# Kernel tuning notes

Hardware: AMD Instinct MI355X
Metric: run time of the kernel (lower is better)

Reference implementation:

```python
import jax, jax.numpy as jnp
import numpy as np

N, C, H, E = 4096, 512, 8, 131072
D = C // H
ALPHA = 0.5
EPS = 1e-5


def layer_norm(x, g, b):
    mu = jnp.mean(x, axis=-1, keepdims=True)
    var = jnp.mean((x - mu) ** 2, axis=-1, keepdims=True)
    return (x - mu) * jax.lax.rsqrt(var + EPS) * g + b


def setup_inputs() -> dict:
    key = jax.random.key(0)
    ks = jax.random.split(key, 20)
    s = 0.02
    return {
        "x": jax.random.normal(ks[0], (N, C), jnp.float32),
        "edge_index": jax.random.randint(ks[1], (2, E), 0, N, jnp.int32),
        "local_w": jax.random.normal(ks[2], (C, C), jnp.float32) * s,
        "local_b": jnp.zeros((C,), jnp.float32),
        "in_proj_w": jax.random.normal(ks[3], (3 * C, C), jnp.float32) * s,
        "in_proj_b": jnp.zeros((3 * C,), jnp.float32),
        "attn_out_w": jax.random.normal(ks[4], (C, C), jnp.float32) * s,
        "attn_out_b": jnp.zeros((C,), jnp.float32),
        "output_w": jax.random.normal(ks[5], (C, C), jnp.float32) * s,
        "output_b": jnp.zeros((C,), jnp.float32),
        "norm1_g": jnp.ones((C,), jnp.float32),
        "norm1_b": jnp.zeros((C,), jnp.float32),
        "norm2_g": jnp.ones((C,), jnp.float32),
        "norm2_b": jnp.zeros((C,), jnp.float32),
        "ffn_w1": jax.random.normal(ks[6], (2 * C, C), jnp.float32) * s,
        "ffn_b1": jnp.zeros((2 * C,), jnp.float32),
        "ffn_w2": jax.random.normal(ks[7], (C, 2 * C), jnp.float32) * s,
        "ffn_b2": jnp.zeros((C,), jnp.float32),
    }


def reference(x, edge_index, local_w, local_b, in_proj_w, in_proj_b,
              attn_out_w, attn_out_b, output_w, output_b,
              norm1_g, norm1_b, norm2_g, norm2_b,
              ffn_w1, ffn_b1, ffn_w2, ffn_b2):
    src, dst = edge_index[0], edge_index[1]

    # local branch: linear then scatter-mean over incoming edges
    local_h = x @ local_w.T + local_b                       # [N,C]
    summed = jax.ops.segment_sum(local_h[src], dst, num_segments=N)
    cnt = jax.ops.segment_sum(jnp.ones((E,), x.dtype), dst, num_segments=N)
    local_out = summed / jnp.maximum(cnt, 1.0)[:, None]

    # global branch: full self-attention over all nodes
    qkv = x @ in_proj_w.T + in_proj_b                       # [N,3C]
    q, k, v = jnp.split(qkv, 3, axis=-1)
    q = q.reshape(N, H, D)
    k = k.reshape(N, H, D)
    v = v.reshape(N, H, D)
    scores = jnp.einsum('nhd,mhd->hnm', q, k) / jnp.sqrt(jnp.asarray(D, x.dtype))
    attn = jax.nn.softmax(scores, axis=-1)                  # [H,N,N]
    ctx = jnp.einsum('hnm,mhd->nhd', attn, v).reshape(N, C)
    global_out = ctx @ attn_out_w.T + attn_out_b

    mixed = ALPHA * local_out + (1.0 - ALPHA) * global_out
    hidden = layer_norm(x + (mixed @ output_w.T + output_b), norm1_g, norm1_b)

    ff = jax.nn.gelu(hidden @ ffn_w1.T + ffn_b1, approximate=False) @ ffn_w2.T + ffn_b2
    return layer_norm(hidden + ff, norm2_g, norm2_b)
```

## Files before the change

kernel.cpp:

```cpp
#include <hip/hip_runtime.h>


#define N_NODES 4096
#define C_DIM   512
#define H_HEADS 8
#define D_HEAD  64
#define E_EDGES 131072

typedef unsigned short u16;
typedef unsigned int   u32;
typedef u16   u16x8  __attribute__((ext_vector_type(8)));
typedef __bf16 bf16x8 __attribute__((ext_vector_type(8)));
typedef float  f32x4  __attribute__((ext_vector_type(4)));

__device__ __forceinline__ float b2f(u16 u) {
  unsigned int i = ((unsigned int)u) << 16;
  return __builtin_bit_cast(float, i);
}
__device__ __forceinline__ u16 f2b(float f) {
  unsigned int i = __builtin_bit_cast(unsigned int, f);
  i += 0x7fffu + ((i >> 16) & 1u);
  return (u16)(i >> 16);
}
__device__ __forceinline__ u16 f2b_up(float f) {
  unsigned int i = __builtin_bit_cast(unsigned int, f);
  return (u16)((i + 0x8000u) >> 16);
}
__device__ __forceinline__ void glds16(const u16* g, u16* l) {
  __builtin_amdgcn_global_load_lds(
      (const __attribute__((address_space(1))) void*)g,
      (__attribute__((address_space(3))) void*)l, 16, 0, 0);
}

struct CvtArgs {
  const float* src[7];
  u16* dst[7];
  int n[7];
  const int* ei;
  int* deg;
};

__global__ __launch_bounds__(256) void cvt_multi(CvtArgs a) {
  const int t = blockIdx.y;
  if (t == 7) {
    if (blockIdx.x >= E_EDGES / 256) return;
    const int e = blockIdx.x * 256 + threadIdx.x;
    atomicAdd(&a.deg[a.ei[E_EDGES + e]], 1);
    return;
  }
  const int i = (blockIdx.x * 256 + threadIdx.x) * 8;
  if (i >= a.n[t]) return;
  const float* s = a.src[t] + i;
  f32x4 v0 = *(const f32x4*)s;
  f32x4 v1 = *(const f32x4*)(s + 4);
  u16x8 o;
  o[0]=f2b(v0[0]); o[1]=f2b(v0[1]); o[2]=f2b(v0[2]); o[3]=f2b(v0[3]);
  o[4]=f2b(v1[0]); o[5]=f2b(v1[1]); o[6]=f2b(v1[2]); o[7]=f2b(v1[3]);
  *(u16x8*)(a.dst[t] + i) = o;
}

template<int EPI>
__global__ __launch_bounds__(256) void gemm_bt(
    const u16* __restrict__ A, const u16* __restrict__ W,
    const float* __restrict__ bias, void* __restrict__ outp,
    int M, int Nout, int K,
    const float* __restrict__ mloc)
{
  const int tid  = threadIdx.x;
  const int lane = tid & 63, wave = tid >> 6;
  const int quad = lane >> 4, l16 = lane & 15;
  const int wm = wave >> 1, wn = wave & 1;
  const int bm = blockIdx.x, bnb = blockIdx.y;

  __shared__ __align__(16) u16 As[64][128];
  __shared__ __align__(16) u16 Ws[64][128];

  f32x4 acc[2][2] = {};

  const int lr4 = lane >> 4, gs = lane & 15;
  const int g8e = (gs ^ lr4) * 8;
  const int g8o = (gs ^ (4 + lr4)) * 8;
  const u16* aw[8];
#pragma unroll
  for (int c = 0; c < 4; ++c) {
    const int g8 = (c & 1) ? g8o : g8e;
    aw[c]     = A + (size_t)(bm  * 64 + wave * 16 + c * 4 + lr4) * K + g8;
    aw[4 + c] = W + (size_t)(bnb * 64 + wave * 16 + c * 4 + lr4) * K + g8;
  }

  for (int k0 = 0; k0 < K; k0 += 128) {
    __syncthreads();
#pragma unroll
    for (int c = 0; c < 4; ++c) {
      glds16(aw[c] + k0,     &As[wave * 16 + c * 4][0]);
      glds16(aw[4 + c] + k0, &Ws[wave * 16 + c * 4][0]);
    }
    __syncthreads();
#pragma unroll
    for (int ks = 0; ks < 4; ++ks) {
      const int slot = ((ks * 4 + quad) ^ (l16 & 7)) * 8;
      bf16x8 af[2], bf[2];
      af[0] = *(const bf16x8*)&As[wm * 32 +      l16][slot];
      af[1] = *(const bf16x8*)&As[wm * 32 + 16 + l16][slot];
      bf[0] = *(const bf16x8*)&Ws[wn * 32 +      l16][slot];
      bf[1] = *(const bf16x8*)&Ws[wn * 32 + 16 + l16][slot];
#pragma unroll
      for (int i = 0; i < 2; ++i)
#pragma unroll
        for (int j = 0; j < 2; ++j)
          acc[i][j] = __builtin_amdgcn_mfma_f32_16x16x32_bf16(af[i], bf[j], acc[i][j], 0, 0, 0);
    }
  }

#pragma unroll
  for (int i = 0; i < 2; ++i)
#pragma unroll
    for (int j = 0; j < 2; ++j) {
      const int col = bnb * 64 + wn * 32 + j * 16 + l16;
      const float bias_v = bias[col];
#pragma unroll
      for (int r = 0; r < 4; ++r) {
        const int row = bm * 64 + wm * 32 + i * 16 + quad * 4 + r;
        float v = acc[i][j][r] + bias_v;
        const size_t o = (size_t)row * Nout + col;
        if constexpr (EPI == 1) {
          ((float*)outp)[o] = v;
        } else if constexpr (EPI == 2) {
          float gl = 0.5f * v * (1.0f + erff(v * 0.70710678118654752f));
          ((u16*)outp)[o] = f2b(gl);
        } else {
          ((u16*)outp)[o] = f2b(0.5f * mloc[o] + 0.5f * v);
        }
      }
    }
}

__global__ __launch_bounds__(256) void gemm128(
    const u16* __restrict__ A, const u16* __restrict__ W,
    const float* __restrict__ bias0, const float* __restrict__ bias1,
    u16* __restrict__ out0, u16* __restrict__ out1,
    int M, int Nout, int K)
{
  const int tid  = threadIdx.x;
  const int lane = tid & 63, wave = tid >> 6;
  const int quad = lane >> 4, l16 = lane & 15;
  const int wm = wave >> 1, wn = wave & 1;
  const int bm = blockIdx.x, bnb = blockIdx.y;

  __shared__ __align__(16) u16 As[128][64];
  __shared__ __align__(16) u16 Ws[128][64];

  f32x4 acc[4][4] = {};

  const int lr = lane >> 3, gs = lane & 7;
  const int g8 = (gs ^ lr) * 8;
  const u16* ab = A + (size_t)(bm  * 128 + wave * 32 + lr) * K + g8;
  const u16* wb = W + (size_t)(bnb * 128 + wave * 32 + lr) * K + g8;

  for (int k0 = 0; k0 < K; k0 += 64) {
    __syncthreads();
#pragma unroll
    for (int c = 0; c < 4; ++c) {
      glds16(ab + (size_t)(c * 8) * K + k0, &As[wave * 32 + c * 8][0]);
      glds16(wb + (size_t)(c * 8) * K + k0, &Ws[wave * 32 + c * 8][0]);
    }
    __syncthreads();
#pragma unroll
    for (int ks = 0; ks < 2; ++ks) {
      const int slot = ((ks * 4 + quad) ^ (l16 & 7)) * 8;
      bf16x8 af[4], bf[4];
#pragma unroll
      for (int am = 0; am < 4; ++am)
        af[am] = *(const bf16x8*)&As[wm * 64 + am * 16 + l16][slot];
#pragma unroll
      for (int bn = 0; bn < 4; ++bn)
        bf[bn] = *(const bf16x8*)&Ws[wn * 64 + bn * 16 + l16][slot];
#pragma unroll
      for (int am = 0; am < 4; ++am)
#pragma unroll
        for (int bn = 0; bn < 4; ++bn)
          acc[am][bn] = __builtin_amdgcn_mfma_f32_16x16x32_bf16(af[am], bf[bn], acc[am][bn], 0, 0, 0);
    }
  }

#pragma unroll
  for (int am = 0; am < 4; ++am)
#pragma unroll
    for (int bn = 0; bn < 4; ++bn) {
      const int col = bnb * 128 + wn * 64 + bn * 16 + l16;
      const float bias_v = (col < 512) ? bias0[col] : bias1[col - 512];
#pragma unroll
      for (int r = 0; r < 4; ++r) {
        const int row = bm * 128 + wm * 64 + am * 16 + quad * 4 + r;
        float v = acc[am][bn][r] + bias_v;
        if (col < 512) out0[(size_t)row * 512 + col] = f2b(v);
        else           out1[(size_t)row * 1536 + (col - 512)] = f2b(v);
      }
    }
}

__global__ __launch_bounds__(256) void scan_kernel(
    const int* __restrict__ deg, int* __restrict__ off, int* __restrict__ cursor)
{
  __shared__ int part[256];
  const int t = threadIdx.x;
  int v[16];
  int s = 0;
#pragma unroll
  for (int i = 0; i < 16; ++i) { v[i] = deg[t * 16 + i]; s += v[i]; }
  part[t] = s;
  __syncthreads();
  for (int d = 1; d < 256; d <<= 1) {
    int val = (t >= d) ? part[t - d] : 0;
    __syncthreads();
    if (t >= d) part[t] += val;
    __syncthreads();
  }
  int prefix = (t == 0) ? 0 : part[t - 1];
#pragma unroll
  for (int i = 0; i < 16; ++i) {
    off[t * 16 + i] = prefix;
    cursor[t * 16 + i] = prefix;
    prefix += v[i];
  }
  if (t == 255) off[4096] = prefix;
}

__global__ __launch_bounds__(256) void fill_kernel(
    const int* __restrict__ ei, int* __restrict__ cursor, int* __restrict__ csr)
{
  const int e = blockIdx.x * 256 + threadIdx.x;
  const int s = ei[e];
  const int d = ei[E_EDGES + e];
  const int p = atomicAdd(&cursor[d], 1);
  csr[p] = s;
}

__global__ __launch_bounds__(256) void gather_vtrans(
    const int* __restrict__ off, const int* __restrict__ csr,
    const u16* __restrict__ lh, float* __restrict__ lo,
    const u16* __restrict__ qkv, u16* __restrict__ vt)
{
  if (blockIdx.y == 0) {
    const int wave = threadIdx.x >> 6, lane = threadIdx.x & 63;
    const int n = blockIdx.x * 4 + wave;
    const int j0 = off[n], j1 = off[n + 1];
    float acc[8] = {};
    for (int j = j0; j < j1; ++j) {
      const int s = csr[j];
      const u16x8 v = *(const u16x8*)(lh + (size_t)s * C_DIM + lane * 8);
#pragma unroll
      for (int i = 0; i < 8; ++i) acc[i] += b2f(v[i]);
    }
    const float inv = 1.0f / fmaxf((float)(j1 - j0), 1.0f);
    f32x4 o0, o1;
#pragma unroll
    for (int i = 0; i < 4; ++i) { o0[i] = acc[i] * inv; o1[i] = acc[4 + i] * inv; }
    float* op = lo + (size_t)n * C_DIM + lane * 8;
    *(f32x4*)op = o0;
    *(f32x4*)(op + 4) = o1;
  } else {
    if (blockIdx.x >= 512) return;
    const int tid = threadIdx.x;
    const int d = tid & 63, mg = tid >> 6;
    const int h = blockIdx.x >> 6, mt = blockIdx.x & 63;
    const int m0 = mt * 64 + mg * 16;
    u16 buf[16];
#pragma unroll
    for (int i = 0; i < 16; ++i)
      buf[i] = qkv[(size_t)(m0 + i) * 1536 + 1024 + h * 64 + d];
    u16x8 w0, w1;
#pragma unroll
    for (int i = 0; i < 8; ++i) { w0[i] = buf[i]; w1[i] = buf[8 + i]; }
    u16* op = vt + (size_t)(h * 64 + d) * N_NODES + m0;
    *(u16x8*)op = w0;
    *(u16x8*)(op + 8) = w1;
  }
}

template<int SPLITS>
__global__ __launch_bounds__(256) void attn_kernel(
    const u16* __restrict__ qkv, const u16* __restrict__ vt,
    u16* __restrict__ opart, float* __restrict__ lpart)
{
  const int tid = threadIdx.x, wave = tid >> 6, lane = tid & 63;
  const int quad = lane >> 4, l16 = lane & 15;
  const int h = blockIdx.y, tile = blockIdx.x, split = blockIdx.z;

  __shared__ __align__(16) u16 Ks[64][64];
  __shared__ __align__(16) u16 Vts[64][64];
  __shared__ __align__(16) u16 Ps[128][72];

  const float QSCALE = 0.18033688011112042f;
  bf16x8 aq[2][2];
#pragma unroll
  for (int mb = 0; mb < 2; ++mb) {
    const int qrow = tile * 128 + wave * 32 + mb * 16 + l16;
    const u16* qp = qkv + (size_t)qrow * 1536 + h * 64 + quad * 8;
    u16x8 q0 = *(const u16x8*)qp;
    u16x8 q1 = *(const u16x8*)(qp + 32);
    u16x8 s0, s1;
#pragma unroll
    for (int i = 0; i < 8; ++i) {
      s0[i] = f2b(b2f(q0[i]) * QSCALE);
      s1[i] = f2b(b2f(q1[i]) * QSCALE);
    }
    aq[mb][0] = __builtin_bit_cast(bf16x8, s0);
    aq[mb][1] = __builtin_bit_cast(bf16x8, s1);
  }

  f32x4 O[2][4] = {};
  float lsum[2][4] = {};

  const int lr = lane >> 3, gs = lane & 7;
  const int g8 = (gs ^ lr) * 8;
  const int R0 = wave * 16 + lr;

  const int mt1 = (split + 1) * (64 / SPLITS);
  for (int mt = split * (64 / SPLITS); mt < mt1; ++mt) {
    __syncthreads();
    glds16(qkv + (size_t)(mt * 64 + R0)     * 1536 + 512 + h * 64 + g8, &Ks[wave * 16][0]);
    glds16(qkv + (size_t)(mt * 64 + R0 + 8) * 1536 + 512 + h * 64 + g8, &Ks[wave * 16 + 8][0]);
    glds16(vt + (size_t)(h * 64 + R0)     * N_NODES + mt * 64 + g8, &Vts[wave * 16][0]);
    glds16(vt + (size_t)(h * 64 + R0 + 8) * N_NODES + mt * 64 + g8, &Vts[wave * 16 + 8][0]);
    __syncthreads();

    f32x4 s[2][4] = {};
#pragma unroll
    for (int ks = 0; ks < 2; ++ks) {
      const int slot = ((ks * 4 + quad) ^ (l16 & 7)) * 8;
      bf16x8 bk[4];
#pragma unroll
      for (int jn = 0; jn < 4; ++jn)
        bk[jn] = *(const bf16x8*)&Ks[jn * 16 + l16][slot];
#pragma unroll
      for (int mb = 0; mb < 2; ++mb)
#pragma unroll
        for (int jn = 0; jn < 4; ++jn)
          s[mb][jn] = __builtin_amdgcn_mfma_f32_16x16x32_bf16(aq[mb][ks], bk[jn], s[mb][jn], 0, 0, 0);
    }

#pragma unroll
    for (int mb = 0; mb < 2; ++mb)
#pragma unroll
      for (int jn = 0; jn < 4; ++jn)
#pragma unroll
        for (int r = 0; r < 4; ++r) {
          float p = __builtin_amdgcn_exp2f(s[mb][jn][r]);
          lsum[mb][r] += p;
          Ps[wave * 32 + mb * 16 + quad * 4 + r][jn * 16 + l16] = f2b_up(p);
        }

#pragma unroll
    for (int ks = 0; ks < 2; ++ks) {
      const int slot = ((ks * 4 + quad) ^ (l16 & 7)) * 8;
      bf16x8 bv[4];
#pragma unroll
      for (int jd = 0; jd < 4; ++jd)
        bv[jd] = *(const bf16x8*)&Vts[jd * 16 + l16][slot];
#pragma unroll
      for (int mb = 0; mb < 2; ++mb) {
        bf16x8 ap = *(const bf16x8*)&Ps[wave * 32 + mb * 16 + l16][ks * 32 + quad * 8];
#pragma unroll
        for (int jd = 0; jd < 4; ++jd)
          O[mb][jd] = __builtin_amdgcn_mfma_f32_16x16x32_bf16(ap, bv[jd], O[mb][jd], 0, 0, 0);
      }
    }
  }

#pragma unroll
  for (int mb = 0; mb < 2; ++mb)
#pragma unroll
    for (int r = 0; r < 4; ++r)
#pragma unroll
      for (int off = 1; off < 16; off <<= 1)
        lsum[mb][r] += __shfl_xor(lsum[mb][r], off);

#pragma unroll
  for (int mb = 0; mb < 2; ++mb)
#pragma unroll
    for (int r = 0; r < 4; ++r) {
      const int row = tile * 128 + wave * 32 + mb * 16 + quad * 4 + r;
      u16* orow = opart + ((size_t)split * N_NODES + row) * C_DIM + h * 64;
#pragma unroll
      for (int jd = 0; jd < 4; ++jd)
        orow[jd * 16 + l16] = f2b(O[mb][jd][r]);
      if (l16 == 0)
        lpart[((size_t)split * N_NODES + row) * H_HEADS + h] = lsum[mb][r];
    }
}

template<int SPLITS>
__global__ __launch_bounds__(256) void attn_combine(
    const u16* __restrict__ opart, const float* __restrict__ lpart,
    u16* __restrict__ ctx)
{
  const size_t base = (size_t)(blockIdx.x * 256 + threadIdx.x) * 8;
  const int row = (int)(base >> 9);
  const int h = (int)((base & 511) >> 6);
  float l = 0.0f;
#pragma unroll
  for (int s = 0; s < SPLITS; ++s)
    l += lpart[(size_t)s * N_NODES * H_HEADS + (size_t)row * H_HEADS + h];
  const float inv = 1.0f / l;
  float o[8] = {};
#pragma unroll
  for (int s = 0; s < SPLITS; ++s) {
    const u16x8 p = *(const u16x8*)(opart + (size_t)s * N_NODES * C_DIM + base);
#pragma unroll
    for (int i = 0; i < 8; ++i) o[i] += b2f(p[i]);
  }
  u16x8 ob;
#pragma unroll
  for (int i = 0; i < 8; ++i) ob[i] = f2b(o[i] * inv);
  *(u16x8*)(ctx + base) = ob;
}

__global__ __launch_bounds__(256) void ln1_kernel(
    const float* __restrict__ x, const float* __restrict__ pr,
    const float* __restrict__ g, const float* __restrict__ b,
    u16* __restrict__ hb, float* __restrict__ hf)
{
  const int wave = threadIdx.x >> 6, lane = threadIdx.x & 63;
  const int row = blockIdx.x * 4 + wave;
  const int c0 = lane * 8;
  const size_t base = (size_t)row * C_DIM + c0;
  f32x4 x0 = *(const f32x4*)(x + base);
  f32x4 x1 = *(const f32x4*)(x + base + 4);
  f32x4 p0 = *(const f32x4*)(pr + base);
  f32x4 p1 = *(const f32x4*)(pr + base + 4);
  float v[8];
#pragma unroll
  for (int i = 0; i < 4; ++i) { v[i] = x0[i] + p0[i]; v[4 + i] = x1[i] + p1[i]; }
  float sum = 0, sq = 0;
#pragma unroll
  for (int i = 0; i < 8; ++i) { sum += v[i]; sq += v[i] * v[i]; }
  for (int off = 1; off < 64; off <<= 1) { sum += __shfl_xor(sum, off); sq += __shfl_xor(sq, off); }
  const float mean = sum * (1.0f / C_DIM);
  const float var  = sq * (1.0f / C_DIM) - mean * mean;
  const float rstd = rsqrtf(var + 1e-5f);
  f32x4 g0 = *(const f32x4*)(g + c0), g1 = *(const f32x4*)(g + c0 + 4);
  f32x4 b0 = *(const f32x4*)(b + c0), b1 = *(const f32x4*)(b + c0 + 4);
  u16x8 ob; f32x4 h0, h1;
#pragma unroll
  for (int i = 0; i < 4; ++i) {
    float hv0 = (v[i]     - mean) * rstd * g0[i] + b0[i];
    float hv1 = (v[4 + i] - mean) * rstd * g1[i] + b1[i];
    h0[i] = hv0; h1[i] = hv1;
    ob[i] = f2b(hv0); ob[4 + i] = f2b(hv1);
  }
  *(u16x8*)(hb + base) = ob;
  *(f32x4*)(hf + base) = h0;
  *(f32x4*)(hf + base + 4) = h1;
}

__global__ __launch_bounds__(256) void ln2_kernel(
    const float* __restrict__ a, const float* __restrict__ c,
    const float* __restrict__ g, const float* __restrict__ b,
    float* __restrict__ out)
{
  const int wave = threadIdx.x >> 6, lane = threadIdx.x & 63;
  const int row = blockIdx.x * 4 + wave;
  const int c0 = lane * 8;
  const size_t base = (size_t)row * C_DIM + c0;
  f32x4 a0 = *(const f32x4*)(a + base), a1 = *(const f32x4*)(a + base + 4);
  f32x4 c0v = *(const f32x4*)(c + base), c1v = *(const f32x4*)(c + base + 4);
  float v[8];
#pragma unroll
  for (int i = 0; i < 4; ++i) { v[i] = a0[i] + c0v[i]; v[4 + i] = a1[i] + c1v[i]; }
  float sum = 0, sq = 0;
#pragma unroll
  for (int i = 0; i < 8; ++i) { sum += v[i]; sq += v[i] * v[i]; }
  for (int off = 1; off < 64; off <<= 1) { sum += __shfl_xor(sum, off); sq += __shfl_xor(sq, off); }
  const float mean = sum * (1.0f / C_DIM);
  const float var  = sq * (1.0f / C_DIM) - mean * mean;
  const float rstd = rsqrtf(var + 1e-5f);
  f32x4 g0 = *(const f32x4*)(g + c0), g1 = *(const f32x4*)(g + c0 + 4);
  f32x4 b0 = *(const f32x4*)(b + c0), b1 = *(const f32x4*)(b + c0 + 4);
  f32x4 h0, h1;
#pragma unroll
  for (int i = 0; i < 4; ++i) {
    h0[i] = (v[i]     - mean) * rstd * g0[i] + b0[i];
    h1[i] = (v[4 + i] - mean) * rstd * g1[i] + b1[i];
  }
  *(f32x4*)(out + base) = h0;
  *(f32x4*)(out + base + 4) = h1;
}

extern "C" void kernel_launch(void* const* d_in, const int* in_sizes, int n_in,
                              void* d_out, int out_size, void* d_ws, size_t ws_size,
                              hipStream_t stream) {
  const float* x          = (const float*)d_in[0];
  const int*   ei         = (const int*)d_in[1];
  const float* local_w    = (const float*)d_in[2];
  const float* local_b    = (const float*)d_in[3];
  const float* in_proj_w  = (const float*)d_in[4];
  const float* in_proj_b  = (const float*)d_in[5];
  const float* attn_out_w = (const float*)d_in[6];
  const float* attn_out_b = (const float*)d_in[7];
  const float* output_w   = (const float*)d_in[8];
  const float* output_b   = (const float*)d_in[9];
  const float* n1g = (const float*)d_in[10];
  const float* n1b = (const float*)d_in[11];
  const float* n2g = (const float*)d_in[12];
  const float* n2b = (const float*)d_in[13];
  const float* ffn_w1 = (const float*)d_in[14];
  const float* ffn_b1 = (const float*)d_in[15];
  const float* ffn_w2 = (const float*)d_in[16];
  const float* ffn_b2 = (const float*)d_in[17];
  float* out = (float*)d_out;

  char* ws = (char*)d_ws;
  size_t o = 0;
  float* local_out = (float*)(ws + o); o += (size_t)N_NODES * C_DIM * 4;
  int* deg    = (int*)(ws + o); o += (N_NODES) * 4;
  int* off    = (int*)(ws + o); o += (N_NODES + 16) * 4;
  int* cursor = (int*)(ws + o); o += (N_NODES) * 4;
  int* csr    = (int*)(ws + o); o += (size_t)E_EDGES * 4;
  u16* xb   = (u16*)(ws + o); o += (size_t)N_NODES * C_DIM * 2;
  u16* wbLQ = (u16*)(ws + o); o += (size_t)4 * C_DIM * C_DIM * 2;
  u16* wbA  = (u16*)(ws + o); o += (size_t)C_DIM * C_DIM * 2;
  u16* wbO  = (u16*)(ws + o); o += (size_t)C_DIM * C_DIM * 2;
  u16* wbF1 = (u16*)(ws + o); o += (size_t)2 * C_DIM * C_DIM * 2;
  u16* wbF2 = (u16*)(ws + o); o += (size_t)2 * C_DIM * C_DIM * 2;
  u16* local_h   = (u16*)(ws + o); o += (size_t)N_NODES * C_DIM * 2;
  u16* qkvb      = (u16*)(ws + o); o += (size_t)N_NODES * 3 * C_DIM * 2;
  u16* ctxb      = (u16*)(ws + o); o += (size_t)N_NODES * C_DIM * 2;
  u16* mixed     = (u16*)(ws + o); o += (size_t)N_NODES * C_DIM * 2;
  u16* hidden_bf = (u16*)(ws + o); o += (size_t)N_NODES * C_DIM * 2;
  float* hidden_f = (float*)(ws + o); o += (size_t)N_NODES * C_DIM * 4;
  u16* ff1       = (u16*)(ws + o); o += (size_t)N_NODES * 2 * C_DIM * 2;
  float* proj  = (float*)qkvb;
  float* ff2   = (float*)local_out;
  u16*   vt    = xb;
  u16* opart4 = (u16*)(ws + o);
  float* lpart4 = (float*)(ws + o + (size_t)4 * N_NODES * C_DIM * 2);
  const size_t need4 = o + (size_t)4 * N_NODES * C_DIM * 2 + (size_t)4 * N_NODES * H_HEADS * 4;
  const bool use4 = (ws_size >= need4);
  u16* opart2 = (u16*)hidden_bf;
  float* lpart2 = (float*)(opart2 + (size_t)2 * N_NODES * C_DIM);

  (void)hipMemsetAsync(deg, 0, N_NODES * 4, stream);

  CvtArgs ca;
  ca.src[0] = x;          ca.dst[0] = xb;   ca.n[0] = N_NODES * C_DIM;
  ca.src[1] = local_w;    ca.dst[1] = wbLQ;                  ca.n[1] = C_DIM * C_DIM;
  ca.src[2] = in_proj_w;  ca.dst[2] = wbLQ + C_DIM * C_DIM;  ca.n[2] = 3 * C_DIM * C_DIM;
  ca.src[3] = attn_out_w; ca.dst[3] = wbA;  ca.n[3] = C_DIM * C_DIM;
  ca.src[4] = output_w;   ca.dst[4] = wbO;  ca.n[4] = C_DIM * C_DIM;
  ca.src[5] = ffn_w1;     ca.dst[5] = wbF1; ca.n[5] = 2 * C_DIM * C_DIM;
  ca.src[6] = ffn_w2;     ca.dst[6] = wbF2; ca.n[6] = 2 * C_DIM * C_DIM;
  ca.ei = ei; ca.deg = deg;
  cvt_multi<<<dim3(N_NODES * C_DIM / 2048, 8), 256, 0, stream>>>(ca);

  scan_kernel<<<1, 256, 0, stream>>>(deg, off, cursor);
  fill_kernel<<<E_EDGES / 256, 256, 0, stream>>>(ei, cursor, csr);

  gemm128<<<dim3(32, 16), 256, 0, stream>>>(xb, wbLQ, local_b, in_proj_b,
      local_h, qkvb, N_NODES, 4 * C_DIM, C_DIM);

  gather_vtrans<<<dim3(N_NODES / 4, 2), 256, 0, stream>>>(off, csr, local_h,
      local_out, qkvb, vt);

  if (use4) {
    attn_kernel<4><<<dim3(32, 8, 4), 256, 0, stream>>>(qkvb, vt, opart4, lpart4);
    attn_combine<4><<<N_NODES * C_DIM / 2048, 256, 0, stream>>>(opart4, lpart4, ctxb);
  } else {
    attn_kernel<2><<<dim3(32, 8, 2), 256, 0, stream>>>(qkvb, vt, opart2, lpart2);
    attn_combine<2><<<N_NODES * C_DIM / 2048, 256, 0, stream>>>(opart2, lpart2, ctxb);
  }

  gemm_bt<3><<<dim3(64, 8), 256, 0, stream>>>(ctxb, wbA, attn_out_b, mixed,
      N_NODES, C_DIM, C_DIM, local_out);

  gemm_bt<1><<<dim3(64, 8), 256, 0, stream>>>(mixed, wbO, output_b, proj,
      N_NODES, C_DIM, C_DIM, nullptr);
  ln1_kernel<<<N_NODES / 4, 256, 0, stream>>>(x, proj, n1g, n1b, hidden_bf, hidden_f);

  gemm_bt<2><<<dim3(64, 16), 256, 0, stream>>>(hidden_bf, wbF1, ffn_b1, ff1,
      N_NODES, 2 * C_DIM, C_DIM, nullptr);
  gemm_bt<1><<<dim3(64, 8), 256, 0, stream>>>(ff1, wbF2, ffn_b2, ff2,
      N_NODES, C_DIM, 2 * C_DIM, nullptr);
  ln2_kernel<<<N_NODES / 4, 256, 0, stream>>>(hidden_f, ff2, n2g, n2b, out);
}
```

Measured before the change: 272.1 us.

## Fold graph CSR build into GEMM, vtrans and attention kernels to cut launches

Moves the degree counting into extra blocks of the QKV GEMM, merges the prefix scan with the V transpose, moves the CSR fill into extra blocks of the attention kernel, and fuses the neighbour gather with the attention combine. The deg memset becomes a block in the conversion kernel. The aim is to drop several small kernel launches and the memset, and to hide the latency-bound graph work behind the large kernels. In exchange the atomic-heavy blocks now compete with the GEMM and attention blocks for the same GPU.

```diff
diff --git a/kernel.cpp b/kernel.cpp
--- a/kernel.cpp
+++ b/kernel.cpp
@@ -36,16 +36,14 @@
   const float* src[7];
   u16* dst[7];
   int n[7];
-  const int* ei;
   int* deg;
 };
 
 __global__ __launch_bounds__(256) void cvt_multi(CvtArgs a) {
   const int t = blockIdx.y;
   if (t == 7) {
-    if (blockIdx.x >= E_EDGES / 256) return;
-    const int e = blockIdx.x * 256 + threadIdx.x;
-    atomicAdd(&a.deg[a.ei[E_EDGES + e]], 1);
+    const int i = blockIdx.x * 256 + threadIdx.x;
+    if (i < N_NODES) a.deg[i] = 0;
     return;
   }
   const int i = (blockIdx.x * 256 + threadIdx.x) * 8;
@@ -139,9 +137,18 @@
     const u16* __restrict__ A, const u16* __restrict__ W,
     const float* __restrict__ bias0, const float* __restrict__ bias1,
     u16* __restrict__ out0, u16* __restrict__ out1,
-    int M, int Nout, int K)
+    int M, int Nout, int K,
+    const int* __restrict__ ei, int* __restrict__ deg)
 {
   const int tid  = threadIdx.x;
+  if (blockIdx.y == 16) {
+#pragma unroll
+    for (int i = 0; i < 16; ++i) {
+      const int e = blockIdx.x * 4096 + i * 256 + tid;
+      atomicAdd(&deg[ei[E_EDGES + e]], 1);
+    }
+    return;
+  }
   const int lane = tid & 63, wave = tid >> 6;
   const int quad = lane >> 4, l16 = lane & 15;
   const int wm = wave >> 1, wn = wave & 1;
@@ -199,47 +206,183 @@
     }
 }
 
-__global__ __launch_bounds__(256) void scan_kernel(
-    const int* __restrict__ deg, int* __restrict__ off, int* __restrict__ cursor)
-{
-  __shared__ int part[256];
-  const int t = threadIdx.x;
-  int v[16];
-  int s = 0;
-#pragma unroll
-  for (int i = 0; i < 16; ++i) { v[i] = deg[t * 16 + i]; s += v[i]; }
-  part[t] = s;
-  __syncthreads();
-  for (int d = 1; d < 256; d <<= 1) {
-    int val = (t >= d) ? part[t - d] : 0;
-    __syncthreads();
-    if (t >= d) part[t] += val;
-    __syncthreads();
-  }
-  int prefix = (t == 0) ? 0 : part[t - 1];
-#pragma unroll
-  for (int i = 0; i < 16; ++i) {
-    off[t * 16 + i] = prefix;
-    cursor[t * 16 + i] = prefix;
-    prefix += v[i];
-  }
-  if (t == 255) off[4096] = prefix;
-}
-
-__global__ __launch_bounds__(256) void fill_kernel(
+__global__ __launch_bounds__(256) void scan_vtrans(
+    const int* __restrict__ deg, int* __restrict__ off, int* __restrict__ cursor,
+    const u16* __restrict__ qkv, u16* __restrict__ vt)
+{
+  if (blockIdx.x == 512) {
+    __shared__ int part[256];
+    const int t = threadIdx.x;
+    int v[16];
+    int s = 0;
+#pragma unroll
+    for (int i = 0; i < 16; ++i) { v[i] = deg[t * 16 + i]; s += v[i]; }
+    part[t] = s;
+    __syncthreads();
+    for (int d = 1; d < 256; d <<= 1) {
+      int val = (t >= d) ? part[t - d] : 0;
+      __syncthreads();
+      if (t >= d) part[t] += val;
+      __syncthreads();
+    }
+    int prefix = (t == 0) ? 0 : part[t - 1];
+#pragma unroll
+    for (int i = 0; i < 16; ++i) {
+      off[t * 16 + i] = prefix;
+      cursor[t * 16 + i] = prefix;
+      prefix += v[i];
+    }
+    if (t == 255) off[4096] = prefix;
+    return;
+  }
+  const int tid = threadIdx.x;
+  const int d = tid & 63, mg = tid >> 6;
+  const int h = blockIdx.x >> 6, mt = blockIdx.x & 63;
+  const int m0 = mt * 64 + mg * 16;
+  u16 buf[16];
+#pragma unroll
+  for (int i = 0; i < 16; ++i)
+    buf[i] = qkv[(size_t)(m0 + i) * 1536 + 1024 + h * 64 + d];
+  u16x8 w0, w1;
+#pragma unroll
+  for (int i = 0; i < 8; ++i) { w0[i] = buf[i]; w1[i] = buf[8 + i]; }
+  u16* op = vt + (size_t)(h * 64 + d) * N_NODES + m0;
+  *(u16x8*)op = w0;
+  *(u16x8*)(op + 8) = w1;
+}
+
+template<int SPLITS>
+__global__ __launch_bounds__(256) void attn_kernel(
+    const u16* __restrict__ qkv, const u16* __restrict__ vt,
+    u16* __restrict__ opart, float* __restrict__ lpart,
     const int* __restrict__ ei, int* __restrict__ cursor, int* __restrict__ csr)
 {
-  const int e = blockIdx.x * 256 + threadIdx.x;
-  const int s = ei[e];
-  const int d = ei[E_EDGES + e];
-  const int p = atomicAdd(&cursor[d], 1);
-  csr[p] = s;
-}
-
-__global__ __launch_bounds__(256) void gather_vtrans(
+  const int tid = threadIdx.x, wave = tid >> 6, lane = tid & 63;
+  const int split = blockIdx.z;
+  if (split == SPLITS) {
+    const int sblk = blockIdx.y * 32 + blockIdx.x;
+#pragma unroll
+    for (int i = 0; i < 2; ++i) {
+      const int e = sblk * 512 + i * 256 + tid;
+      const int s = ei[e];
+      const int d = ei[E_EDGES + e];
+      const int p = atomicAdd(&cursor[d], 1);
+      csr[p] = s;
+    }
+    return;
+  }
+  const int quad = lane >> 4, l16 = lane & 15;
+  const int h = blockIdx.y, tile = blockIdx.x;
+
+  __shared__ __align__(16) u16 Ks[64][64];
+  __shared__ __align__(16) u16 Vts[64][64];
+  __shared__ __align__(16) u16 Ps[128][72];
+
+  const float QSCALE = 0.18033688011112042f;
+  bf16x8 aq[2][2];
+#pragma unroll
+  for (int mb = 0; mb < 2; ++mb) {
+    const int qrow = tile * 128 + wave * 32 + mb * 16 + l16;
+    const u16* qp = qkv + (size_t)qrow * 1536 + h * 64 + quad * 8;
+    u16x8 q0 = *(const u16x8*)qp;
+    u16x8 q1 = *(const u16x8*)(qp + 32);
+    u16x8 s0, s1;
+#pragma unroll
+    for (int i = 0; i < 8; ++i) {
+      s0[i] = f2b(b2f(q0[i]) * QSCALE);
+      s1[i] = f2b(b2f(q1[i]) * QSCALE);
+    }
+    aq[mb][0] = __builtin_bit_cast(bf16x8, s0);
+    aq[mb][1] = __builtin_bit_cast(bf16x8, s1);
+  }
+
+  f32x4 O[2][4] = {};
+  float lsum[2][4] = {};
+
+  const int lr = lane >> 3, gs = lane & 7;
+  const int g8 = (gs ^ lr) * 8;
+  const int R0 = wave * 16 + lr;
+
+  const int mt1 = (split + 1) * (64 / SPLITS);
+  for (int mt = split * (64 / SPLITS); mt < mt1; ++mt) {
+    __syncthreads();
+    glds16(qkv + (size_t)(mt * 64 + R0)     * 1536 + 512 + h * 64 + g8, &Ks[wave * 16][0]);
+    glds16(qkv + (size_t)(mt * 64 + R0 + 8) * 1536 + 512 + h * 64 + g8, &Ks[wave * 16 + 8][0]);
+    glds16(vt + (size_t)(h * 64 + R0)     * N_NODES + mt * 64 + g8, &Vts[wave * 16][0]);
+    glds16(vt + (size_t)(h * 64 + R0 + 8) * N_NODES + mt * 64 + g8, &Vts[wave * 16 + 8][0]);
+    __syncthreads();
+
+    f32x4 s[2][4] = {};
+#pragma unroll
+    for (int ks = 0; ks < 2; ++ks) {
+      const int slot = ((ks * 4 + quad) ^ (l16 & 7)) * 8;
+      bf16x8 bk[4];
+#pragma unroll
+      for (int jn = 0; jn < 4; ++jn)
+        bk[jn] = *(const bf16x8*)&Ks[jn * 16 + l16][slot];
+#pragma unroll
+      for (int mb = 0; mb < 2; ++mb)
+#pragma unroll
+        for (int jn = 0; jn < 4; ++jn)
+          s[mb][jn] = __builtin_amdgcn_mfma_f32_16x16x32_bf16(aq[mb][ks], bk[jn], s[mb][jn], 0, 0, 0);
+    }
+
+#pragma unroll
+    for (int mb = 0; mb < 2; ++mb)
+#pragma unroll
+      for (int jn = 0; jn < 4; ++jn)
+#pragma unroll
+        for (int r = 0; r < 4; ++r) {
+          float p = __builtin_amdgcn_exp2f(s[mb][jn][r]);
+          lsum[mb][r] += p;
+          Ps[wave * 32 + mb * 16 + quad * 4 + r][jn * 16 + l16] = f2b_up(p);
+        }
+
+#pragma unroll
+    for (int ks = 0; ks < 2; ++ks) {
+      const int slot = ((ks * 4 + quad) ^ (l16 & 7)) * 8;
+      bf16x8 bv[4];
+#pragma unroll
+      for (int jd = 0; jd < 4; ++jd)
+        bv[jd] = *(const bf16x8*)&Vts[jd * 16 + l16][slot];
+#pragma unroll
+      for (int mb = 0; mb < 2; ++mb) {
+        bf16x8 ap = *(const bf16x8*)&Ps[wave * 32 + mb * 16 + l16][ks * 32 + quad * 8];
+#pragma unroll
+        for (int jd = 0; jd < 4; ++jd)
+          O[mb][jd] = __builtin_amdgcn_mfma_f32_16x16x32_bf16(ap, bv[jd], O[mb][jd], 0, 0, 0);
+      }
+    }
+  }
+
+#pragma unroll
+  for (int mb = 0; mb < 2; ++mb)
+#pragma unroll
+    for (int r = 0; r < 4; ++r)
+#pragma unroll
+      for (int off = 1; off < 16; off <<= 1)
+        lsum[mb][r] += __shfl_xor(lsum[mb][r], off);
+
+#pragma unroll
+  for (int mb = 0; mb < 2; ++mb)
+#pragma unroll
+    for (int r = 0; r < 4; ++r) {
+      const int row = tile * 128 + wave * 32 + mb * 16 + quad * 4 + r;
+      u16* orow = opart + ((size_t)split * N_NODES + row) * C_DIM + h * 64;
+#pragma unroll
+      for (int jd = 0; jd < 4; ++jd)
+        orow[jd * 16 + l16] = f2b(O[mb][jd][r]);
+      if (l16 == 0)
+        lpart[((size_t)split * N_NODES + row) * H_HEADS + h] = lsum[mb][r];
+    }
+}
+
+template<int SPLITS>
+__global__ __launch_bounds__(256) void combine_gather(
+    const u16* __restrict__ opart, const float* __restrict__ lpart,
+    u16* __restrict__ ctx,
     const int* __restrict__ off, const int* __restrict__ csr,
-    const u16* __restrict__ lh, float* __restrict__ lo,
-    const u16* __restrict__ qkv, u16* __restrict__ vt)
+    const u16* __restrict__ lh, float* __restrict__ lo)
 {
   if (blockIdx.y == 0) {
     const int wave = threadIdx.x >> 6, lane = threadIdx.x & 63;
@@ -259,142 +402,8 @@
     float* op = lo + (size_t)n * C_DIM + lane * 8;
     *(f32x4*)op = o0;
     *(f32x4*)(op + 4) = o1;
-  } else {
-    if (blockIdx.x >= 512) return;
-    const int tid = threadIdx.x;
-    const int d = tid & 63, mg = tid >> 6;
-    const int h = blockIdx.x >> 6, mt = blockIdx.x & 63;
-    const int m0 = mt * 64 + mg * 16;
-    u16 buf[16];
-#pragma unroll
-    for (int i = 0; i < 16; ++i)
-      buf[i] = qkv[(size_t)(m0 + i) * 1536 + 1024 + h * 64 + d];
-    u16x8 w0, w1;
-#pragma unroll
-    for (int i = 0; i < 8; ++i) { w0[i] = buf[i]; w1[i] = buf[8 + i]; }
-    u16* op = vt + (size_t)(h * 64 + d) * N_NODES + m0;
-    *(u16x8*)op = w0;
-    *(u16x8*)(op + 8) = w1;
-  }
-}
-
-template<int SPLITS>
-__global__ __launch_bounds__(256) void attn_kernel(
-    const u16* __restrict__ qkv, const u16* __restrict__ vt,
-    u16* __restrict__ opart, float* __restrict__ lpart)
-{
-  const int tid = threadIdx.x, wave = tid >> 6, lane = tid & 63;
-  const int quad = lane >> 4, l16 = lane & 15;
-  const int h = blockIdx.y, tile = blockIdx.x, split = blockIdx.z;
-
-  __shared__ __align__(16) u16 Ks[64][64];
-  __shared__ __align__(16) u16 Vts[64][64];
-  __shared__ __align__(16) u16 Ps[128][72];
-
-  const float QSCALE = 0.18033688011112042f;
-  bf16x8 aq[2][2];
-#pragma unroll
-  for (int mb = 0; mb < 2; ++mb) {
-    const int qrow = tile * 128 + wave * 32 + mb * 16 + l16;
-    const u16* qp = qkv + (size_t)qrow * 1536 + h * 64 + quad * 8;
-    u16x8 q0 = *(const u16x8*)qp;
-    u16x8 q1 = *(const u16x8*)(qp + 32);
-    u16x8 s0, s1;
-#pragma unroll
-    for (int i = 0; i < 8; ++i) {
-      s0[i] = f2b(b2f(q0[i]) * QSCALE);
-      s1[i] = f2b(b2f(q1[i]) * QSCALE);
-    }
-    aq[mb][0] = __builtin_bit_cast(bf16x8, s0);
-    aq[mb][1] = __builtin_bit_cast(bf16x8, s1);
-  }
-
-  f32x4 O[2][4] = {};
-  float lsum[2][4] = {};
-
-  const int lr = lane >> 3, gs = lane & 7;
-  const int g8 = (gs ^ lr) * 8;
-  const int R0 = wave * 16 + lr;
-
-  const int mt1 = (split + 1) * (64 / SPLITS);
-  for (int mt = split * (64 / SPLITS); mt < mt1; ++mt) {
-    __syncthreads();
-    glds16(qkv + (size_t)(mt * 64 + R0)     * 1536 + 512 + h * 64 + g8, &Ks[wave * 16][0]);
-    glds16(qkv + (size_t)(mt * 64 + R0 + 8) * 1536 + 512 + h * 64 + g8, &Ks[wave * 16 + 8][0]);
-    glds16(vt + (size_t)(h * 64 + R0)     * N_NODES + mt * 64 + g8, &Vts[wave * 16][0]);
-    glds16(vt + (size_t)(h * 64 + R0 + 8) * N_NODES + mt * 64 + g8, &Vts[wave * 16 + 8][0]);
-    __syncthreads();
-
-    f32x4 s[2][4] = {};
-#pragma unroll
-    for (int ks = 0; ks < 2; ++ks) {
-      const int slot = ((ks * 4 + quad) ^ (l16 & 7)) * 8;
-      bf16x8 bk[4];
-#pragma unroll
-      for (int jn = 0; jn < 4; ++jn)
-        bk[jn] = *(const bf16x8*)&Ks[jn * 16 + l16][slot];
-#pragma unroll
-      for (int mb = 0; mb < 2; ++mb)
-#pragma unroll
-        for (int jn = 0; jn < 4; ++jn)
-          s[mb][jn] = __builtin_amdgcn_mfma_f32_16x16x32_bf16(aq[mb][ks], bk[jn], s[mb][jn], 0, 0, 0);
-    }
-
-#pragma unroll
-    for (int mb = 0; mb < 2; ++mb)
-#pragma unroll
-      for (int jn = 0; jn < 4; ++jn)
-#pragma unroll
-        for (int r = 0; r < 4; ++r) {
-          float p = __builtin_amdgcn_exp2f(s[mb][jn][r]);
-          lsum[mb][r] += p;
-          Ps[wave * 32 + mb * 16 + quad * 4 + r][jn * 16 + l16] = f2b_up(p);
-        }
-
-#pragma unroll
-    for (int ks = 0; ks < 2; ++ks) {
-      const int slot = ((ks * 4 + quad) ^ (l16 & 7)) * 8;
-      bf16x8 bv[4];
-#pragma unroll
-      for (int jd = 0; jd < 4; ++jd)
-        bv[jd] = *(const bf16x8*)&Vts[jd * 16 + l16][slot];
-#pragma unroll
-      for (int mb = 0; mb < 2; ++mb) {
-        bf16x8 ap = *(const bf16x8*)&Ps[wave * 32 + mb * 16 + l16][ks * 32 + quad * 8];
-#pragma unroll
-        for (int jd = 0; jd < 4; ++jd)
-          O[mb][jd] = __builtin_amdgcn_mfma_f32_16x16x32_bf16(ap, bv[jd], O[mb][jd], 0, 0, 0);
-      }
-    }
-  }
-
-#pragma unroll
-  for (int mb = 0; mb < 2; ++mb)
-#pragma unroll
-    for (int r = 0; r < 4; ++r)
-#pragma unroll
-      for (int off = 1; off < 16; off <<= 1)
-        lsum[mb][r] += __shfl_xor(lsum[mb][r], off);
-
-#pragma unroll
-  for (int mb = 0; mb < 2; ++mb)
-#pragma unroll
-    for (int r = 0; r < 4; ++r) {
-      const int row = tile * 128 + wave * 32 + mb * 16 + quad * 4 + r;
-      u16* orow = opart + ((size_t)split * N_NODES + row) * C_DIM + h * 64;
-#pragma unroll
-      for (int jd = 0; jd < 4; ++jd)
-        orow[jd * 16 + l16] = f2b(O[mb][jd][r]);
-      if (l16 == 0)
-        lpart[((size_t)split * N_NODES + row) * H_HEADS + h] = lsum[mb][r];
-    }
-}
-
-template<int SPLITS>
-__global__ __launch_bounds__(256) void attn_combine(
-    const u16* __restrict__ opart, const float* __restrict__ lpart,
-    u16* __restrict__ ctx)
-{
+    return;
+  }
   const size_t base = (size_t)(blockIdx.x * 256 + threadIdx.x) * 8;
   const int row = (int)(base >> 9);
   const int h = (int)((base & 511) >> 6);
@@ -540,8 +549,6 @@
   u16* opart2 = (u16*)hidden_bf;
   float* lpart2 = (float*)(opart2 + (size_t)2 * N_NODES * C_DIM);
 
-  (void)hipMemsetAsync(deg, 0, N_NODES * 4, stream);
-
   CvtArgs ca;
   ca.src[0] = x;          ca.dst[0] = xb;   ca.n[0] = N_NODES * C_DIM;
   ca.src[1] = local_w;    ca.dst[1] = wbLQ;                  ca.n[1] = C_DIM * C_DIM;
@@ -550,24 +557,24 @@
   ca.src[4] = output_w;   ca.dst[4] = wbO;  ca.n[4] = C_DIM * C_DIM;
   ca.src[5] = ffn_w1;     ca.dst[5] = wbF1; ca.n[5] = 2 * C_DIM * C_DIM;
   ca.src[6] = ffn_w2;     ca.dst[6] = wbF2; ca.n[6] = 2 * C_DIM * C_DIM;
-  ca.ei = ei; ca.deg = deg;
+  ca.deg = deg;
   cvt_multi<<<dim3(N_NODES * C_DIM / 2048, 8), 256, 0, stream>>>(ca);
 
-  scan_kernel<<<1, 256, 0, stream>>>(deg, off, cursor);
-  fill_kernel<<<E_EDGES / 256, 256, 0, stream>>>(ei, cursor, csr);
-
-  gemm128<<<dim3(32, 16), 256, 0, stream>>>(xb, wbLQ, local_b, in_proj_b,
-      local_h, qkvb, N_NODES, 4 * C_DIM, C_DIM);
-
-  gather_vtrans<<<dim3(N_NODES / 4, 2), 256, 0, stream>>>(off, csr, local_h,
-      local_out, qkvb, vt);
+  gemm128<<<dim3(32, 17), 256, 0, stream>>>(xb, wbLQ, local_b, in_proj_b,
+      local_h, qkvb, N_NODES, 4 * C_DIM, C_DIM, ei, deg);
+
+  scan_vtrans<<<513, 256, 0, stream>>>(deg, off, cursor, qkvb, vt);
 
   if (use4) {
-    attn_kernel<4><<<dim3(32, 8, 4), 256, 0, stream>>>(qkvb, vt, opart4, lpart4);
-    attn_combine<4><<<N_NODES * C_DIM / 2048, 256, 0, stream>>>(opart4, lpart4, ctxb);
+    attn_kernel<4><<<dim3(32, 8, 5), 256, 0, stream>>>(qkvb, vt, opart4, lpart4,
+        ei, cursor, csr);
+    combine_gather<4><<<dim3(1024, 2), 256, 0, stream>>>(opart4, lpart4, ctxb,
+        off, csr, local_h, local_out);
   } else {
-    attn_kernel<2><<<dim3(32, 8, 2), 256, 0, stream>>>(qkvb, vt, opart2, lpart2);
-    attn_combine<2><<<N_NODES * C_DIM / 2048, 256, 0, stream>>>(opart2, lpart2, ctxb);
+    attn_kernel<2><<<dim3(32, 8, 3), 256, 0, stream>>>(qkvb, vt, opart2, lpart2,
+        ei, cursor, csr);
+    combine_gather<2><<<dim3(1024, 2), 256, 0, stream>>>(opart2, lpart2, ctxb,
+        off, csr, local_h, local_out);
   }
 
   gemm_bt<3><<<dim3(64, 8), 256, 0, stream>>>(ctxb, wbA, attn_out_b, mixed,
```

Result: faster. 264.2 us (-2.9%).
